# Performance work log

Measured on AMD Instinct MI355X. Metric: run time of the kernel, lower is better.

## Reference

```python
import jax, jax.numpy as jnp
import numpy as np

N_NODES = 100000
N_EDGES = 1600000
HID = 256
HEADS = 4
HEAD_DIM = HID // HEADS
EPS = 1e-5


def _layernorm(x, g, b):
    mu = jnp.mean(x, axis=-1, keepdims=True)
    var = jnp.mean(jnp.square(x - mu), axis=-1, keepdims=True)
    return (x - mu) * jax.lax.rsqrt(var + EPS) * g + b


def setup_inputs() -> dict:
    key = jax.random.key(0)
    ks = jax.random.split(key, 16)
    s = 0.05  # small init, mimics xavier gain=0.1
    inp = {
        'h': jax.random.normal(ks[0], (N_NODES, HID), jnp.float32),
        'src': jax.random.randint(ks[1], (N_EDGES,), 0, N_NODES, jnp.int32),
        'dst': jax.random.randint(ks[2], (N_EDGES,), 0, N_NODES, jnp.int32),
        'Wq': jax.random.normal(ks[3], (HID, HID), jnp.float32) * s,
        'bq': jnp.zeros((HID,), jnp.float32),
        'Wk': jax.random.normal(ks[4], (HID, HID), jnp.float32) * s,
        'bk': jnp.zeros((HID,), jnp.float32),
        'Wv': jax.random.normal(ks[5], (HID, HID), jnp.float32) * s,
        'bv': jnp.zeros((HID,), jnp.float32),
        'Wo': jax.random.normal(ks[6], (HID, HID), jnp.float32) * s,
        'bo': jnp.zeros((HID,), jnp.float32),
        'W1': jax.random.normal(ks[7], (HID, 2 * HID), jnp.float32) * s,
        'b1': jnp.zeros((2 * HID,), jnp.float32),
        'W2': jax.random.normal(ks[8], (2 * HID, HID), jnp.float32) * s,
        'b2': jnp.zeros((HID,), jnp.float32),
        'g1': jnp.ones((HID,), jnp.float32),
        'be1': jnp.zeros((HID,), jnp.float32),
        'g2': jnp.ones((HID,), jnp.float32),
        'be2': jnp.zeros((HID,), jnp.float32),
    }
    return inp


def reference(h, src, dst, Wq, bq, Wk, bk, Wv, bv, Wo, bo, W1, b1, W2, b2, g1, be1, g2, be2):
    N = h.shape[0]
    scale = HEAD_DIM ** -0.5
    h_norm = _layernorm(h, g1, be1)
    Q = (h_norm @ Wq + bq).reshape(N, HEADS, HEAD_DIM)
    K = (h_norm @ Wk + bk).reshape(N, HEADS, HEAD_DIM)
    V = (h_norm @ Wv + bv).reshape(N, HEADS, HEAD_DIM)

    # per-edge attention logits: q from dst, k from src  -> [E, heads]
    logits = jnp.einsum('ehd,ehd->eh', Q[dst], K[src]) * scale

    # edge softmax grouped by destination node (dgl.ops.edge_softmax)
    seg_max = jax.ops.segment_max(logits, dst, num_segments=N)  # [N, heads]
    e = jnp.exp(logits - seg_max[dst])
    seg_sum = jax.ops.segment_sum(e, dst, num_segments=N)
    w = e / seg_sum[dst]  # [E, heads]

    # message = V[src] * attn ; aggregate by sum over incoming edges
    msg = V[src] * w[:, :, None]  # [E, heads, head_dim]
    h_new = jax.ops.segment_sum(msg, dst, num_segments=N).reshape(N, HID)

    h_attn = h_new @ Wo + bo
    h = h + h_attn  # dropout is identity in eval
    h2 = _layernorm(h, g2, be2)
    ffn = jax.nn.relu(h2 @ W1 + b1) @ W2 + b2
    return h + ffn
```

## Files before the change

### kernel.cpp

```cpp
#include <hip/hip_runtime.h>
#include <hip/hip_bf16.h>

#define NN 100000
#define NE 1600000

typedef __attribute__((ext_vector_type(8))) short bf16x8;
typedef __attribute__((ext_vector_type(4))) float f32x4;
typedef __attribute__((ext_vector_type(2))) float f32x2;
typedef __attribute__((ext_vector_type(2))) unsigned int u32x2;
typedef __attribute__((ext_vector_type(4))) unsigned int u32x4;

__device__ __forceinline__ float bf2f(unsigned short u) {
    union { unsigned int i; float f; } c; c.i = ((unsigned int)u) << 16; return c.f;
}
__device__ __forceinline__ unsigned short f2bf(float f) {
    union { float f; unsigned int i; } c; c.f = f;
    unsigned int lsb = (c.i >> 16) & 1u;
    c.i += 0x7FFFu + lsb;
    return (unsigned short)(c.i >> 16);
}
__device__ __forceinline__ u32x4 pack8bf(f32x4 a, f32x4 b) {
    u32x4 p;
    p.x = f2bf(a[0]) | ((unsigned int)f2bf(a[1]) << 16);
    p.y = f2bf(a[2]) | ((unsigned int)f2bf(a[3]) << 16);
    p.z = f2bf(b[0]) | ((unsigned int)f2bf(b[1]) << 16);
    p.w = f2bf(b[2]) | ((unsigned int)f2bf(b[3]) << 16);
    return p;
}
__device__ __forceinline__ void gload_lds16(const void* g, void* l) {
    __builtin_amdgcn_global_load_lds(
        (const __attribute__((address_space(1))) void*)g,
        (__attribute__((address_space(3))) void*)l, 16, 0, 0);
}

__global__ __launch_bounds__(256) void ln_k(
    const float* __restrict__ x, const float* __restrict__ g,
    const float* __restrict__ b, unsigned short* __restrict__ y, int nrows)
{
    int w = threadIdx.x >> 6, lane = threadIdx.x & 63;
    int row = blockIdx.x * 4 + w;
    if (row >= nrows) return;
    const float4 xv = *(const float4*)(x + (size_t)row * 256 + lane * 4);
    float s  = xv.x + xv.y + xv.z + xv.w;
    float sq = xv.x*xv.x + xv.y*xv.y + xv.z*xv.z + xv.w*xv.w;
    #pragma unroll
    for (int m = 1; m < 64; m <<= 1) {
        s  += __shfl_xor(s,  m);
        sq += __shfl_xor(sq, m);
    }
    float mu  = s * (1.0f / 256.0f);
    float var = sq * (1.0f / 256.0f) - mu * mu;
    float r = rsqrtf(var + 1e-5f);
    float4 gv = *(const float4*)(g + lane * 4);
    float4 bv = *(const float4*)(b + lane * 4);
    ushort4 o;
    o.x = f2bf((xv.x - mu) * r * gv.x + bv.x);
    o.y = f2bf((xv.y - mu) * r * gv.y + bv.y);
    o.z = f2bf((xv.z - mu) * r * gv.z + bv.z);
    o.w = f2bf((xv.w - mu) * r * gv.w + bv.w);
    *(ushort4*)(y + (size_t)row * 256 + lane * 4) = o;
}

__global__ __launch_bounds__(256) void wconv_k(
    const float* __restrict__ W, unsigned short* __restrict__ Wt, int K, int N)
{
    __shared__ unsigned short tl[32][33];
    int bk = blockIdx.x * 32, bn = blockIdx.y * 32;
    int lx = threadIdx.x & 31, ly = threadIdx.x >> 5;
    #pragma unroll
    for (int r = 0; r < 32; r += 8)
        tl[ly + r][lx] = f2bf(W[(size_t)(bk + ly + r) * N + bn + lx]);
    __syncthreads();
    #pragma unroll
    for (int r = 0; r < 32; r += 8)
        Wt[(size_t)(bn + ly + r) * K + bk + lx] = tl[lx][ly + r];
}

__global__ void bcat_k(const float* __restrict__ a, const float* __restrict__ b,
                       const float* __restrict__ c, float* __restrict__ o)
{
    int t = threadIdx.x;
    o[t] = a[t]; o[256 + t] = b[t]; o[512 + t] = c[t];
}

template<int OMODE, bool RELU, bool RES>
__global__ __launch_bounds__(512) void mgemm_k(
    const unsigned short* __restrict__ A, const unsigned short* __restrict__ Wt,
    const float* __restrict__ bias, void* __restrict__ outv, void* __restrict__ out2,
    const void* __restrict__ res, const float* __restrict__ g, const float* __restrict__ be,
    int M, int N, int K)
{
    __shared__ __align__(16) char lds[49152];
    const int t = threadIdx.x;
    const int lane = t & 63;
    const int wid = t >> 6;
    const int wm = wid >> 2, wn = wid & 3;
    const int bm = blockIdx.y * 128, bn = blockIdx.x * 256;

    f32x4 acc[4][4] = {};

    const int ra_s = t >> 2;
    const int sa_s = (t & 3) ^ (ra_s & 3);
    const size_t arow = (size_t)min(bm + ra_s, M - 1) * K + sa_s * 8;
    const int rb0 = t >> 2;
    const int sb0 = (t & 3) ^ (rb0 & 3);
    const int rb1 = (512 + t) >> 2;
    const int sb1 = (t & 3) ^ (rb1 & 3);
    const size_t brow0 = (size_t)(bn + rb0) * K + sb0 * 8;
    const size_t brow1 = (size_t)(bn + rb1) * K + sb1 * 8;

    const int fr = lane & 15, fs = lane >> 4;
    const int rslot = fs ^ (fr & 3);

    const int KS = K >> 5;
    int cur = 0;
    {
        unsigned short* Ab = (unsigned short*)(lds);
        unsigned short* Bb = (unsigned short*)(lds + 16384);
        gload_lds16(A + arow, Ab + t * 8);
        gload_lds16(Wt + brow0, Bb + t * 8);
        gload_lds16(Wt + brow1, Bb + (512 + t) * 8);
    }
    for (int ks = 0; ks < KS; ++ks) {
        __syncthreads();
        if (ks + 1 < KS) {
            int k1 = (ks + 1) << 5;
            unsigned short* Ab = (unsigned short*)(lds + (cur ^ 1) * 8192);
            unsigned short* Bb = (unsigned short*)(lds + 16384 + (cur ^ 1) * 16384);
            gload_lds16(A + arow + k1, Ab + t * 8);
            gload_lds16(Wt + brow0 + k1, Bb + t * 8);
            gload_lds16(Wt + brow1 + k1, Bb + (512 + t) * 8);
        }
        const unsigned short* As = (const unsigned short*)(lds + cur * 8192);
        const unsigned short* Bs = (const unsigned short*)(lds + 16384 + cur * 16384);
        bf16x8 af[4], bf[4];
        #pragma unroll
        for (int fm = 0; fm < 4; ++fm)
            af[fm] = *(const bf16x8*)&As[(wm * 64 + fm * 16 + fr) * 32 + rslot * 8];
        #pragma unroll
        for (int fn = 0; fn < 4; ++fn)
            bf[fn] = *(const bf16x8*)&Bs[(wn * 64 + fn * 16 + fr) * 32 + rslot * 8];
        #pragma unroll
        for (int fm = 0; fm < 4; ++fm)
            #pragma unroll
            for (int fn = 0; fn < 4; ++fn)
                acc[fm][fn] = __builtin_amdgcn_mfma_f32_16x16x32_bf16(
                    af[fm], bf[fn], acc[fm][fn], 0, 0, 0);
        cur ^= 1;
    }
    __syncthreads();

    float* wl = (float*)(lds + wid * 4352);
    float* stats = (float*)(lds + 34816);
    const int rr = lane >> 2;
    const int c4 = (lane & 3) * 16;
    const int qg = lane >> 4;

    #pragma unroll
    for (int fm = 0; fm < 4; ++fm) {
        #pragma unroll
        for (int fn = 0; fn < 4; ++fn)
            #pragma unroll
            for (int i = 0; i < 4; ++i)
                wl[(qg * 4 + i) * 68 + fn * 16 + fr] = acc[fm][fn][i];
        f32x4 v0 = *(const f32x4*)&wl[rr * 68 + c4 + 0];
        f32x4 v1 = *(const f32x4*)&wl[rr * 68 + c4 + 4];
        f32x4 v2 = *(const f32x4*)&wl[rr * 68 + c4 + 8];
        f32x4 v3 = *(const f32x4*)&wl[rr * 68 + c4 + 12];
        const int rowg = bm + wm * 64 + fm * 16 + rr;
        const int colg = bn + wn * 64 + c4;
        if (rowg < M) {
            v0 += *(const f32x4*)&bias[colg + 0];
            v1 += *(const f32x4*)&bias[colg + 4];
            v2 += *(const f32x4*)&bias[colg + 8];
            v3 += *(const f32x4*)&bias[colg + 12];
            if (RES) {
                if (OMODE == 4) {
                    const unsigned short* rp = (const unsigned short*)res + (size_t)rowg * N + colg;
                    u32x4 ra = *(const u32x4*)rp;
                    u32x4 rb = *(const u32x4*)(rp + 8);
                    v0[0] += bf2f(ra.x & 0xffff); v0[1] += bf2f(ra.x >> 16);
                    v0[2] += bf2f(ra.y & 0xffff); v0[3] += bf2f(ra.y >> 16);
                    v1[0] += bf2f(ra.z & 0xffff); v1[1] += bf2f(ra.z >> 16);
                    v1[2] += bf2f(ra.w & 0xffff); v1[3] += bf2f(ra.w >> 16);
                    v2[0] += bf2f(rb.x & 0xffff); v2[1] += bf2f(rb.x >> 16);
                    v2[2] += bf2f(rb.y & 0xffff); v2[3] += bf2f(rb.y >> 16);
                    v3[0] += bf2f(rb.z & 0xffff); v3[1] += bf2f(rb.z >> 16);
                    v3[2] += bf2f(rb.w & 0xffff); v3[3] += bf2f(rb.w >> 16);
                } else {
                    const float* rp = (const float*)res + (size_t)rowg * N + colg;
                    v0 += *(const f32x4*)(rp + 0);
                    v1 += *(const f32x4*)(rp + 4);
                    v2 += *(const f32x4*)(rp + 8);
                    v3 += *(const f32x4*)(rp + 12);
                }
            }
            if (RELU) {
                #pragma unroll
                for (int j = 0; j < 4; ++j) {
                    v0[j] = fmaxf(v0[j], 0.f); v1[j] = fmaxf(v1[j], 0.f);
                    v2[j] = fmaxf(v2[j], 0.f); v3[j] = fmaxf(v3[j], 0.f);
                }
            }
        } else {
            v0 = 0.f; v1 = 0.f; v2 = 0.f; v3 = 0.f;
        }

        if (OMODE == 3) {
            acc[fm][0] = v0; acc[fm][1] = v1; acc[fm][2] = v2; acc[fm][3] = v3;
        } else if (rowg < M) {
            if (OMODE == 0 || OMODE == 4) {
                float* op = (float*)outv + (size_t)rowg * N + colg;
                *(f32x4*)(op + 0) = v0; *(f32x4*)(op + 4) = v1;
                *(f32x4*)(op + 8) = v2; *(f32x4*)(op + 12) = v3;
            } else if (OMODE == 1) {
                unsigned short* op = (unsigned short*)outv + (size_t)rowg * N + colg;
                *(u32x4*)(op + 0) = pack8bf(v0, v1);
                *(u32x4*)(op + 8) = pack8bf(v2, v3);
            } else {
                if (colg < 256) {
                    unsigned short* op = (unsigned short*)outv + (size_t)rowg * 256 + colg;
                    *(u32x4*)(op + 0) = pack8bf(v0, v1);
                    *(u32x4*)(op + 8) = pack8bf(v2, v3);
                } else {
                    u32x4 p8;
                    unsigned int w0, w1, w2, w3;
                    w0 = __builtin_amdgcn_cvt_pk_fp8_f32(v0[0], v0[1], 0, false);
                    w0 = __builtin_amdgcn_cvt_pk_fp8_f32(v0[2], v0[3], w0, true);
                    w1 = __builtin_amdgcn_cvt_pk_fp8_f32(v1[0], v1[1], 0, false);
                    w1 = __builtin_amdgcn_cvt_pk_fp8_f32(v1[2], v1[3], w1, true);
                    w2 = __builtin_amdgcn_cvt_pk_fp8_f32(v2[0], v2[1], 0, false);
                    w2 = __builtin_amdgcn_cvt_pk_fp8_f32(v2[2], v2[3], w2, true);
                    w3 = __builtin_amdgcn_cvt_pk_fp8_f32(v3[0], v3[1], 0, false);
                    w3 = __builtin_amdgcn_cvt_pk_fp8_f32(v3[2], v3[3], w3, true);
                    p8.x = w0; p8.y = w1; p8.z = w2; p8.w = w3;
                    *(u32x4*)((unsigned char*)out2 + (size_t)rowg * 512 + (colg - 256)) = p8;
                }
            }
        }
    }

    if (OMODE == 3) {
        #pragma unroll
        for (int fm = 0; fm < 4; ++fm) {
            float s = 0.f, q = 0.f;
            #pragma unroll
            for (int j = 0; j < 4; ++j)
                #pragma unroll
                for (int c = 0; c < 4; ++c) {
                    float x = acc[fm][j][c];
                    s += x; q += x * x;
                }
            s += __shfl_xor(s, 1); q += __shfl_xor(q, 1);
            s += __shfl_xor(s, 2); q += __shfl_xor(q, 2);
            if ((lane & 3) == 0) {
                int rowl = wm * 64 + fm * 16 + rr;
                stats[rowl * 8 + wn * 2 + 0] = s;
                stats[rowl * 8 + wn * 2 + 1] = q;
            }
        }
        __syncthreads();
        #pragma unroll
        for (int fm = 0; fm < 4; ++fm) {
            const int rowl = wm * 64 + fm * 16 + rr;
            const int rowg = bm + rowl;
            float s = stats[rowl * 8 + 0] + stats[rowl * 8 + 2] + stats[rowl * 8 + 4] + stats[rowl * 8 + 6];
            float q = stats[rowl * 8 + 1] + stats[rowl * 8 + 3] + stats[rowl * 8 + 5] + stats[rowl * 8 + 7];
            float mu = s * (1.0f / 256.0f);
            float var = q * (1.0f / 256.0f) - mu * mu;
            float rstd = rsqrtf(var + 1e-5f);
            const int colg = bn + wn * 64 + c4;
            if (rowg < M) {
                unsigned short* mp = (unsigned short*)out2 + (size_t)rowg * 256 + colg;
                *(u32x4*)(mp + 0) = pack8bf(acc[fm][0], acc[fm][1]);
                *(u32x4*)(mp + 8) = pack8bf(acc[fm][2], acc[fm][3]);
                f32x4 nv[4];
                #pragma unroll
                for (int j = 0; j < 4; ++j) {
                    f32x4 gv = *(const f32x4*)&g[colg + j * 4];
                    f32x4 bv = *(const f32x4*)&be[colg + j * 4];
                    #pragma unroll
                    for (int c = 0; c < 4; ++c)
                        nv[j][c] = (acc[fm][j][c] - mu) * rstd * gv[c] + bv[c];
                }
                unsigned short* op = (unsigned short*)outv + (size_t)rowg * 256 + colg;
                *(u32x4*)(op + 0) = pack8bf(nv[0], nv[1]);
                *(u32x4*)(op + 8) = pack8bf(nv[2], nv[3]);
            }
        }
    }
}

__global__ void degcnt_k(const int* __restrict__ dst, int* __restrict__ deg, int E)
{
    int e = blockIdx.x * blockDim.x + threadIdx.x;
    if (e < E) atomicAdd(deg + dst[e], 1);
}

__global__ __launch_bounds__(1024) void scan_k(int* __restrict__ a, int n)
{
    __shared__ int wsum[16];
    __shared__ int carry;
    __shared__ int tot;
    int t = threadIdx.x, lane = t & 63, w = t >> 6;
    if (t == 0) carry = 0;
    __syncthreads();
    for (int base = 0; base < n; base += 1024) {
        int i = base + t;
        int v = (i < n) ? a[i] : 0;
        int s = v;
        #pragma unroll
        for (int d2 = 1; d2 < 64; d2 <<= 1) {
            int u = __shfl_up(s, d2);
            if (lane >= d2) s += u;
        }
        if (lane == 63) wsum[w] = s;
        __syncthreads();
        if (t == 0) {
            int run = 0;
            #pragma unroll
            for (int j = 0; j < 16; ++j) { int x = wsum[j]; wsum[j] = run; run += x; }
            tot = run;
        }
        __syncthreads();
        int excl = carry + wsum[w] + (s - v);
        if (i < n) a[i] = excl;
        __syncthreads();
        if (t == 0) carry += tot;
        __syncthreads();
    }
    if (threadIdx.x == 0) a[n] = carry;
}

__global__ void scatter_k(
    const int* __restrict__ dst, const int* __restrict__ srcarr,
    const int* __restrict__ off, int* __restrict__ cursor,
    int* __restrict__ csr, int E)
{
    int e = blockIdx.x * blockDim.x + threadIdx.x;
    if (e >= E) return;
    int d = dst[e];
    int pos = off[d] + atomicAdd(cursor + d, 1);
    csr[pos] = srcarr[e];
}

__global__ __launch_bounds__(256) void attn_k(
    const int* __restrict__ csr, const int* __restrict__ off,
    const unsigned short* __restrict__ Q, const unsigned char* __restrict__ KV8,
    unsigned short* __restrict__ hnew)
{
    int w = threadIdx.x >> 6, lane = threadIdx.x & 63;
    int n = blockIdx.x * 4 + w;
    if (n >= NN) return;
    int e0 = off[n], e1 = off[n + 1];

    u32x2 qr = __builtin_nontemporal_load((const u32x2*)(Q + (size_t)n * 256 + lane * 4));
    const float q0 = bf2f((unsigned short)(qr.x & 0xffff)) * 0.125f;
    const float q1 = bf2f((unsigned short)(qr.x >> 16))    * 0.125f;
    const float q2 = bf2f((unsigned short)(qr.y & 0xffff)) * 0.125f;
    const float q3 = bf2f((unsigned short)(qr.y >> 16))    * 0.125f;

    float s = 0.f;
    float a0 = 0.f, a1 = 0.f, a2 = 0.f, a3 = 0.f;

    int i = e0;
    for (; i + 7 < e1; i += 8) {
        int ns[8];
        #pragma unroll
        for (int j = 0; j < 8; ++j) ns[j] = csr[i + j];
        unsigned int kd[8], vd[8];
        #pragma unroll
        for (int j = 0; j < 8; ++j) {
            const unsigned char* r = KV8 + (size_t)ns[j] * 512 + lane * 4;
            kd[j] = *(const unsigned int*)r;
            vd[j] = *(const unsigned int*)(r + 256);
        }
        float l[8];
        #pragma unroll
        for (int j = 0; j < 8; ++j) {
            f32x2 ka = __builtin_amdgcn_cvt_pk_f32_fp8(kd[j], false);
            f32x2 kb = __builtin_amdgcn_cvt_pk_f32_fp8(kd[j], true);
            l[j] = q0 * ka.x + q1 * ka.y + q2 * kb.x + q3 * kb.y;
        }
        #pragma unroll
        for (int m2 = 1; m2 < 16; m2 <<= 1) {
            #pragma unroll
            for (int j = 0; j < 8; ++j) l[j] += __shfl_xor(l[j], m2);
        }
        #pragma unroll
        for (int j = 0; j < 8; ++j) {
            float p = __expf(l[j]);
            f32x2 va = __builtin_amdgcn_cvt_pk_f32_fp8(vd[j], false);
            f32x2 vb = __builtin_amdgcn_cvt_pk_f32_fp8(vd[j], true);
            s  += p;
            a0 += p * va.x; a1 += p * va.y;
            a2 += p * vb.x; a3 += p * vb.y;
        }
    }
    for (; i + 3 < e1; i += 4) {
        int ns[4];
        #pragma unroll
        for (int j = 0; j < 4; ++j) ns[j] = csr[i + j];
        unsigned int kd[4], vd[4];
        #pragma unroll
        for (int j = 0; j < 4; ++j) {
            const unsigned char* r = KV8 + (size_t)ns[j] * 512 + lane * 4;
            kd[j] = *(const unsigned int*)r;
            vd[j] = *(const unsigned int*)(r + 256);
        }
        float l[4];
        #pragma unroll
        for (int j = 0; j < 4; ++j) {
            f32x2 ka = __builtin_amdgcn_cvt_pk_f32_fp8(kd[j], false);
            f32x2 kb = __builtin_amdgcn_cvt_pk_f32_fp8(kd[j], true);
            l[j] = q0 * ka.x + q1 * ka.y + q2 * kb.x + q3 * kb.y;
        }
        #pragma unroll
        for (int m2 = 1; m2 < 16; m2 <<= 1) {
            #pragma unroll
            for (int j = 0; j < 4; ++j) l[j] += __shfl_xor(l[j], m2);
        }
        #pragma unroll
        for (int j = 0; j < 4; ++j) {
            float p = __expf(l[j]);
            f32x2 va = __builtin_amdgcn_cvt_pk_f32_fp8(vd[j], false);
            f32x2 vb = __builtin_amdgcn_cvt_pk_f32_fp8(vd[j], true);
            s  += p;
            a0 += p * va.x; a1 += p * va.y;
            a2 += p * vb.x; a3 += p * vb.y;
        }
    }
    for (; i < e1; ++i) {
        int n0 = csr[i];
        const unsigned char* r = KV8 + (size_t)n0 * 512 + lane * 4;
        unsigned int kd = *(const unsigned int*)r;
        unsigned int vd = *(const unsigned int*)(r + 256);
        f32x2 ka = __builtin_amdgcn_cvt_pk_f32_fp8(kd, false);
        f32x2 kb = __builtin_amdgcn_cvt_pk_f32_fp8(kd, true);
        float l0 = q0 * ka.x + q1 * ka.y + q2 * kb.x + q3 * kb.y;
        #pragma unroll
        for (int m2 = 1; m2 < 16; m2 <<= 1) l0 += __shfl_xor(l0, m2);
        float p = __expf(l0);
        f32x2 va = __builtin_amdgcn_cvt_pk_f32_fp8(vd, false);
        f32x2 vb = __builtin_amdgcn_cvt_pk_f32_fp8(vd, true);
        s  += p;
        a0 += p * va.x; a1 += p * va.y;
        a2 += p * vb.x; a3 += p * vb.y;
    }
    float inv = (e1 > e0) ? 1.0f / s : 0.f;
    u32x2 ov;
    ov.x = ((unsigned int)f2bf(a1 * inv) << 16) | f2bf(a0 * inv);
    ov.y = ((unsigned int)f2bf(a3 * inv) << 16) | f2bf(a2 * inv);
    __builtin_nontemporal_store(ov, (u32x2*)(hnew + (size_t)n * 256 + lane * 4));
}

extern "C" void kernel_launch(void* const* d_in, const int* in_sizes, int n_in,
                              void* d_out, int out_size, void* d_ws, size_t ws_size,
                              hipStream_t stream)
{
    if (n_in < 19) return;
    const float* h   = (const float*)d_in[0];
    const int*   src = (const int*)d_in[1];
    const int*   dst = (const int*)d_in[2];
    const float* Wq  = (const float*)d_in[3];
    const float* bq  = (const float*)d_in[4];
    const float* Wk  = (const float*)d_in[5];
    const float* bk  = (const float*)d_in[6];
    const float* Wv  = (const float*)d_in[7];
    const float* bv  = (const float*)d_in[8];
    const float* Wo  = (const float*)d_in[9];
    const float* bo  = (const float*)d_in[10];
    const float* W1  = (const float*)d_in[11];
    const float* b1  = (const float*)d_in[12];
    const float* W2  = (const float*)d_in[13];
    const float* b2  = (const float*)d_in[14];
    const float* g1  = (const float*)d_in[15];
    const float* be1 = (const float*)d_in[16];
    const float* g2  = (const float*)d_in[17];
    const float* be2 = (const float*)d_in[18];
    float* out = (float*)d_out;

    char* w = (char*)d_ws;
    unsigned short* hnormb = (unsigned short*)(w + 0);
    unsigned short* Qb     = (unsigned short*)(w + 51200000);
    unsigned char*  KV8    = (unsigned char*)(w + 102400000);
    int*            degoff = (int*)(w + 153600000);
    int*            cursor = (int*)(w + 154000384);
    int*            csr    = (int*)(w + 154400768);
    unsigned short* Wqkvt  = (unsigned short*)(w + 204800000);
    unsigned short* Wot    = (unsigned short*)(w + 205193216);
    unsigned short* W1t    = (unsigned short*)(w + 205324288);
    unsigned short* W2t    = (unsigned short*)(w + 205586432);
    float*          bqkv   = (float*)(w + 205848576);
    unsigned short* hnewb  = hnormb;
    unsigned short* h2nb   = hnormb;
    unsigned short* hmidb  = Qb;
    unsigned short* ffnmid = (unsigned short*)(w + 102400000);

    hipMemsetAsync(degoff, 0, 400384, stream);
    hipMemsetAsync(cursor, 0, 400384, stream);

    const int M = NN;
    dim3 blk(256);
    dim3 blk512(512);

    wconv_k<<<dim3(8, 8),  blk, 0, stream>>>(Wq, Wqkvt,             256, 256);
    wconv_k<<<dim3(8, 8),  blk, 0, stream>>>(Wk, Wqkvt + 256 * 256, 256, 256);
    wconv_k<<<dim3(8, 8),  blk, 0, stream>>>(Wv, Wqkvt + 512 * 256, 256, 256);
    wconv_k<<<dim3(8, 8),  blk, 0, stream>>>(Wo, Wot, 256, 256);
    wconv_k<<<dim3(8, 16), blk, 0, stream>>>(W1, W1t, 256, 512);
    wconv_k<<<dim3(16, 8), blk, 0, stream>>>(W2, W2t, 512, 256);
    bcat_k<<<dim3(1), blk, 0, stream>>>(bq, bk, bv, bqkv);

    degcnt_k<<<dim3((NE + 255) / 256), blk, 0, stream>>>(dst, degoff, NE);
    scan_k<<<dim3(1), dim3(1024), 0, stream>>>(degoff, NN);
    scatter_k<<<dim3((NE + 255) / 256), blk, 0, stream>>>(dst, src, degoff, cursor, csr, NE);

    ln_k<<<dim3((NN + 3) / 4), blk, 0, stream>>>(h, g1, be1, hnormb, NN);

    dim3 gq(768 / 256, (M + 127) / 128);
    mgemm_k<2, false, false><<<gq, blk512, 0, stream>>>(hnormb, Wqkvt, bqkv, Qb, KV8, nullptr, nullptr, nullptr, M, 768, 256);

    attn_k<<<dim3((NN + 3) / 4), blk, 0, stream>>>(csr, degoff, Qb, KV8, hnewb);

    dim3 go(1, (M + 127) / 128);
    mgemm_k<3, false, true><<<go, blk512, 0, stream>>>(hnewb, Wot, bo, h2nb, hmidb, h, g2, be2, M, 256, 256);

    dim3 g1x(512 / 256, (M + 127) / 128);
    mgemm_k<1, true, false><<<g1x, blk512, 0, stream>>>(h2nb, W1t, b1, ffnmid, nullptr, nullptr, nullptr, nullptr, M, 512, 256);
    mgemm_k<4, false, true><<<go, blk512, 0, stream>>>(ffnmid, W2t, b2, out, nullptr, hmidb, nullptr, nullptr, M, 256, 512);
}
```

Before: 684.2 us.

## Load GEMM fragments directly from global, parallelize scan, fuse weight conversions

The GEMM drops its LDS double-buffered staging: each wave now reads its MFMA fragments straight from global memory with a compile-time K loop that is fully unrolled. It also gains a launch-bounds occupancy hint and keeps LDS only for the epilogue. The single-block degree scan becomes a three-kernel multi-block scan, and the six weight-transpose launches plus the bias concat are merged into one kernel. In attention, the CSR entries are stored as pre-shifted byte offsets and exp is replaced by exp2 with log2(e) folded into the query scale. The risk is that global fragment loads lose the shared reuse across waves and may be less coalesced, which could make the GEMMs more bandwidth-bound.

```diff
diff --git a/kernel.cpp b/kernel.cpp
--- a/kernel.cpp
+++ b/kernel.cpp
@@ -26,11 +26,6 @@
     p.z = f2bf(b[0]) | ((unsigned int)f2bf(b[1]) << 16);
     p.w = f2bf(b[2]) | ((unsigned int)f2bf(b[3]) << 16);
     return p;
-}
-__device__ __forceinline__ void gload_lds16(const void* g, void* l) {
-    __builtin_amdgcn_global_load_lds(
-        (const __attribute__((address_space(1))) void*)g,
-        (__attribute__((address_space(3))) void*)l, 16, 0, 0);
 }
 
 __global__ __launch_bounds__(256) void ln_k(
@@ -61,94 +56,86 @@
     *(ushort4*)(y + (size_t)row * 256 + lane * 4) = o;
 }
 
-__global__ __launch_bounds__(256) void wconv_k(
-    const float* __restrict__ W, unsigned short* __restrict__ Wt, int K, int N)
-{
+__global__ __launch_bounds__(256) void wcv_all_k(
+    const float* __restrict__ Wq, const float* __restrict__ Wk, const float* __restrict__ Wv,
+    const float* __restrict__ Wo, const float* __restrict__ W1, const float* __restrict__ W2,
+    unsigned short* __restrict__ Wqkvt, unsigned short* __restrict__ Wot,
+    unsigned short* __restrict__ W1t, unsigned short* __restrict__ W2t,
+    const float* __restrict__ bq, const float* __restrict__ bk, const float* __restrict__ bv,
+    float* __restrict__ bqkv)
+{
+    int id = blockIdx.x;
+    int t = threadIdx.x;
+    if (id == 512) {
+        bqkv[t] = bq[t]; bqkv[256 + t] = bk[t]; bqkv[512 + t] = bv[t];
+        return;
+    }
+    const float* W; unsigned short* Wt; int K, N, kx, ny;
+    if (id < 192) {
+        int grp = id >> 6, l = id & 63;
+        W = (grp == 0) ? Wq : ((grp == 1) ? Wk : Wv);
+        Wt = Wqkvt + grp * 256 * 256;
+        K = 256; N = 256; kx = l & 7; ny = l >> 3;
+    } else if (id < 256) {
+        int l = id - 192; W = Wo; Wt = Wot; K = 256; N = 256; kx = l & 7; ny = l >> 3;
+    } else if (id < 384) {
+        int l = id - 256; W = W1; Wt = W1t; K = 256; N = 512; kx = l & 7; ny = l >> 3;
+    } else {
+        int l = id - 384; W = W2; Wt = W2t; K = 512; N = 256; kx = l & 15; ny = l >> 4;
+    }
     __shared__ unsigned short tl[32][33];
-    int bk = blockIdx.x * 32, bn = blockIdx.y * 32;
-    int lx = threadIdx.x & 31, ly = threadIdx.x >> 5;
+    int bk2 = kx * 32, bn = ny * 32;
+    int lx = t & 31, ly = t >> 5;
     #pragma unroll
     for (int r = 0; r < 32; r += 8)
-        tl[ly + r][lx] = f2bf(W[(size_t)(bk + ly + r) * N + bn + lx]);
+        tl[ly + r][lx] = f2bf(W[(size_t)(bk2 + ly + r) * N + bn + lx]);
     __syncthreads();
     #pragma unroll
     for (int r = 0; r < 32; r += 8)
-        Wt[(size_t)(bn + ly + r) * K + bk + lx] = tl[lx][ly + r];
-}
-
-__global__ void bcat_k(const float* __restrict__ a, const float* __restrict__ b,
-                       const float* __restrict__ c, float* __restrict__ o)
-{
-    int t = threadIdx.x;
-    o[t] = a[t]; o[256 + t] = b[t]; o[512 + t] = c[t];
-}
-
-template<int OMODE, bool RELU, bool RES>
-__global__ __launch_bounds__(512) void mgemm_k(
+        Wt[(size_t)(bn + ly + r) * K + bk2 + lx] = tl[lx][ly + r];
+}
+
+template<int KS, int OMODE, bool RELU, bool RES>
+__global__ __launch_bounds__(512, 4) void mgemm_k(
     const unsigned short* __restrict__ A, const unsigned short* __restrict__ Wt,
     const float* __restrict__ bias, void* __restrict__ outv, void* __restrict__ out2,
     const void* __restrict__ res, const float* __restrict__ g, const float* __restrict__ be,
-    int M, int N, int K)
-{
-    __shared__ __align__(16) char lds[49152];
+    int M, int N)
+{
+    constexpr int K = KS * 32;
+    __shared__ __align__(16) char lds[38912];
     const int t = threadIdx.x;
     const int lane = t & 63;
     const int wid = t >> 6;
     const int wm = wid >> 2, wn = wid & 3;
     const int bm = blockIdx.y * 128, bn = blockIdx.x * 256;
+    const int fr = lane & 15, fs = lane >> 4;
 
     f32x4 acc[4][4] = {};
 
-    const int ra_s = t >> 2;
-    const int sa_s = (t & 3) ^ (ra_s & 3);
-    const size_t arow = (size_t)min(bm + ra_s, M - 1) * K + sa_s * 8;
-    const int rb0 = t >> 2;
-    const int sb0 = (t & 3) ^ (rb0 & 3);
-    const int rb1 = (512 + t) >> 2;
-    const int sb1 = (t & 3) ^ (rb1 & 3);
-    const size_t brow0 = (size_t)(bn + rb0) * K + sb0 * 8;
-    const size_t brow1 = (size_t)(bn + rb1) * K + sb1 * 8;
-
-    const int fr = lane & 15, fs = lane >> 4;
-    const int rslot = fs ^ (fr & 3);
-
-    const int KS = K >> 5;
-    int cur = 0;
-    {
-        unsigned short* Ab = (unsigned short*)(lds);
-        unsigned short* Bb = (unsigned short*)(lds + 16384);
-        gload_lds16(A + arow, Ab + t * 8);
-        gload_lds16(Wt + brow0, Bb + t * 8);
-        gload_lds16(Wt + brow1, Bb + (512 + t) * 8);
-    }
+    const unsigned short* Ap[4];
+    const unsigned short* Bp[4];
+    #pragma unroll
+    for (int fm = 0; fm < 4; ++fm)
+        Ap[fm] = A + (size_t)min(bm + wm * 64 + fm * 16 + fr, M - 1) * K + fs * 8;
+    #pragma unroll
+    for (int fn = 0; fn < 4; ++fn)
+        Bp[fn] = Wt + (size_t)(bn + wn * 64 + fn * 16 + fr) * K + fs * 8;
+
+    #pragma unroll
     for (int ks = 0; ks < KS; ++ks) {
-        __syncthreads();
-        if (ks + 1 < KS) {
-            int k1 = (ks + 1) << 5;
-            unsigned short* Ab = (unsigned short*)(lds + (cur ^ 1) * 8192);
-            unsigned short* Bb = (unsigned short*)(lds + 16384 + (cur ^ 1) * 16384);
-            gload_lds16(A + arow + k1, Ab + t * 8);
-            gload_lds16(Wt + brow0 + k1, Bb + t * 8);
-            gload_lds16(Wt + brow1 + k1, Bb + (512 + t) * 8);
-        }
-        const unsigned short* As = (const unsigned short*)(lds + cur * 8192);
-        const unsigned short* Bs = (const unsigned short*)(lds + 16384 + cur * 16384);
         bf16x8 af[4], bf[4];
         #pragma unroll
-        for (int fm = 0; fm < 4; ++fm)
-            af[fm] = *(const bf16x8*)&As[(wm * 64 + fm * 16 + fr) * 32 + rslot * 8];
-        #pragma unroll
-        for (int fn = 0; fn < 4; ++fn)
-            bf[fn] = *(const bf16x8*)&Bs[(wn * 64 + fn * 16 + fr) * 32 + rslot * 8];
+        for (int fm = 0; fm < 4; ++fm) af[fm] = *(const bf16x8*)(Ap[fm] + ks * 32);
+        #pragma unroll
+        for (int fn = 0; fn < 4; ++fn) bf[fn] = *(const bf16x8*)(Bp[fn] + ks * 32);
         #pragma unroll
         for (int fm = 0; fm < 4; ++fm)
             #pragma unroll
             for (int fn = 0; fn < 4; ++fn)
                 acc[fm][fn] = __builtin_amdgcn_mfma_f32_16x16x32_bf16(
                     af[fm], bf[fn], acc[fm][fn], 0, 0, 0);
-        cur ^= 1;
-    }
-    __syncthreads();
+    }
 
     float* wl = (float*)(lds + wid * 4352);
     float* stats = (float*)(lds + 34816);
@@ -163,6 +150,7 @@
             #pragma unroll
             for (int i = 0; i < 4; ++i)
                 wl[(qg * 4 + i) * 68 + fn * 16 + fr] = acc[fm][fn][i];
+        __builtin_amdgcn_s_waitcnt(0);
         f32x4 v0 = *(const f32x4*)&wl[rr * 68 + c4 + 0];
         f32x4 v1 = *(const f32x4*)&wl[rr * 68 + c4 + 4];
         f32x4 v2 = *(const f32x4*)&wl[rr * 68 + c4 + 8];
@@ -297,39 +285,53 @@
     if (e < E) atomicAdd(deg + dst[e], 1);
 }
 
-__global__ __launch_bounds__(1024) void scan_k(int* __restrict__ a, int n)
+__global__ __launch_bounds__(1024) void scanA_k(int* __restrict__ a, int* __restrict__ aux, int n)
 {
     __shared__ int wsum[16];
-    __shared__ int carry;
-    __shared__ int tot;
+    __shared__ int wpre[16];
     int t = threadIdx.x, lane = t & 63, w = t >> 6;
-    if (t == 0) carry = 0;
+    int i = blockIdx.x * 1024 + t;
+    int v = (i < n) ? a[i] : 0;
+    int s = v;
+    #pragma unroll
+    for (int d = 1; d < 64; d <<= 1) {
+        int u = __shfl_up(s, d);
+        if (lane >= d) s += u;
+    }
+    if (lane == 63) wsum[w] = s;
     __syncthreads();
-    for (int base = 0; base < n; base += 1024) {
-        int i = base + t;
-        int v = (i < n) ? a[i] : 0;
-        int s = v;
-        #pragma unroll
-        for (int d2 = 1; d2 < 64; d2 <<= 1) {
-            int u = __shfl_up(s, d2);
-            if (lane >= d2) s += u;
-        }
-        if (lane == 63) wsum[w] = s;
-        __syncthreads();
-        if (t == 0) {
-            int run = 0;
-            #pragma unroll
-            for (int j = 0; j < 16; ++j) { int x = wsum[j]; wsum[j] = run; run += x; }
-            tot = run;
-        }
-        __syncthreads();
-        int excl = carry + wsum[w] + (s - v);
-        if (i < n) a[i] = excl;
-        __syncthreads();
-        if (t == 0) carry += tot;
-        __syncthreads();
-    }
-    if (threadIdx.x == 0) a[n] = carry;
+    if (t == 0) {
+        int run = 0;
+        #pragma unroll
+        for (int j = 0; j < 16; ++j) { wpre[j] = run; run += wsum[j]; }
+        aux[blockIdx.x] = run;
+    }
+    __syncthreads();
+    if (i < n) a[i] = wpre[w] + s - v;
+}
+
+__global__ __launch_bounds__(128) void scanB_k(int* __restrict__ aux, int* __restrict__ tot, int nb)
+{
+    __shared__ int ws[2];
+    int t = threadIdx.x, lane = t & 63, w = t >> 6;
+    int v = (t < nb) ? aux[t] : 0;
+    int s = v;
+    #pragma unroll
+    for (int d = 1; d < 64; d <<= 1) {
+        int u = __shfl_up(s, d);
+        if (lane >= d) s += u;
+    }
+    if (lane == 63) ws[w] = s;
+    __syncthreads();
+    int add = (w == 1) ? ws[0] : 0;
+    if (t < nb) aux[t] = add + s - v;
+    if (t == nb - 1) tot[0] = add + s;
+}
+
+__global__ __launch_bounds__(1024) void scanC_k(int* __restrict__ a, const int* __restrict__ aux, int n)
+{
+    int i = blockIdx.x * 1024 + threadIdx.x;
+    if (i < n) a[i] += aux[blockIdx.x];
 }
 
 __global__ void scatter_k(
@@ -341,7 +343,7 @@
     if (e >= E) return;
     int d = dst[e];
     int pos = off[d] + atomicAdd(cursor + d, 1);
-    csr[pos] = srcarr[e];
+    csr[pos] = srcarr[e] << 9;
 }
 
 __global__ __launch_bounds__(256) void attn_k(
@@ -354,11 +356,14 @@
     if (n >= NN) return;
     int e0 = off[n], e1 = off[n + 1];
 
+    const unsigned char* KVl = KV8 + lane * 4;
+
     u32x2 qr = __builtin_nontemporal_load((const u32x2*)(Q + (size_t)n * 256 + lane * 4));
-    const float q0 = bf2f((unsigned short)(qr.x & 0xffff)) * 0.125f;
-    const float q1 = bf2f((unsigned short)(qr.x >> 16))    * 0.125f;
-    const float q2 = bf2f((unsigned short)(qr.y & 0xffff)) * 0.125f;
-    const float q3 = bf2f((unsigned short)(qr.y >> 16))    * 0.125f;
+    const float qs = 0.125f * 1.4426950408889634f;
+    const float q0 = bf2f((unsigned short)(qr.x & 0xffff)) * qs;
+    const float q1 = bf2f((unsigned short)(qr.x >> 16))    * qs;
+    const float q2 = bf2f((unsigned short)(qr.y & 0xffff)) * qs;
+    const float q3 = bf2f((unsigned short)(qr.y >> 16))    * qs;
 
     float s = 0.f;
     float a0 = 0.f, a1 = 0.f, a2 = 0.f, a3 = 0.f;
@@ -371,7 +376,7 @@
         unsigned int kd[8], vd[8];
         #pragma unroll
         for (int j = 0; j < 8; ++j) {
-            const unsigned char* r = KV8 + (size_t)ns[j] * 512 + lane * 4;
+            const unsigned char* r = KVl + (size_t)(unsigned)ns[j];
             kd[j] = *(const unsigned int*)r;
             vd[j] = *(const unsigned int*)(r + 256);
         }
@@ -389,7 +394,7 @@
         }
         #pragma unroll
         for (int j = 0; j < 8; ++j) {
-            float p = __expf(l[j]);
+            float p = exp2f(l[j]);
             f32x2 va = __builtin_amdgcn_cvt_pk_f32_fp8(vd[j], false);
             f32x2 vb = __builtin_amdgcn_cvt_pk_f32_fp8(vd[j], true);
             s  += p;
@@ -404,7 +409,7 @@
         unsigned int kd[4], vd[4];
         #pragma unroll
         for (int j = 0; j < 4; ++j) {
-            const unsigned char* r = KV8 + (size_t)ns[j] * 512 + lane * 4;
+            const unsigned char* r = KVl + (size_t)(unsigned)ns[j];
             kd[j] = *(const unsigned int*)r;
             vd[j] = *(const unsigned int*)(r + 256);
         }
@@ -422,7 +427,7 @@
         }
         #pragma unroll
         for (int j = 0; j < 4; ++j) {
-            float p = __expf(l[j]);
+            float p = exp2f(l[j]);
             f32x2 va = __builtin_amdgcn_cvt_pk_f32_fp8(vd[j], false);
             f32x2 vb = __builtin_amdgcn_cvt_pk_f32_fp8(vd[j], true);
             s  += p;
@@ -431,8 +436,7 @@
         }
     }
     for (; i < e1; ++i) {
-        int n0 = csr[i];
-        const unsigned char* r = KV8 + (size_t)n0 * 512 + lane * 4;
+        const unsigned char* r = KVl + (size_t)(unsigned)csr[i];
         unsigned int kd = *(const unsigned int*)r;
         unsigned int vd = *(const unsigned int*)(r + 256);
         f32x2 ka = __builtin_amdgcn_cvt_pk_f32_fp8(kd, false);
@@ -440,7 +444,7 @@
         float l0 = q0 * ka.x + q1 * ka.y + q2 * kb.x + q3 * kb.y;
         #pragma unroll
         for (int m2 = 1; m2 < 16; m2 <<= 1) l0 += __shfl_xor(l0, m2);
-        float p = __expf(l0);
+        float p = exp2f(l0);
         f32x2 va = __builtin_amdgcn_cvt_pk_f32_fp8(vd, false);
         f32x2 vb = __builtin_amdgcn_cvt_pk_f32_fp8(vd, true);
         s  += p;
@@ -492,6 +496,7 @@
     unsigned short* W1t    = (unsigned short*)(w + 205324288);
     unsigned short* W2t    = (unsigned short*)(w + 205586432);
     float*          bqkv   = (float*)(w + 205848576);
+    int*            scanaux= (int*)(w + 205851648);
     unsigned short* hnewb  = hnormb;
     unsigned short* h2nb   = hnormb;
     unsigned short* hmidb  = Qb;
@@ -503,30 +508,28 @@
     const int M = NN;
     dim3 blk(256);
     dim3 blk512(512);
-
-    wconv_k<<<dim3(8, 8),  blk, 0, stream>>>(Wq, Wqkvt,             256, 256);
-    wconv_k<<<dim3(8, 8),  blk, 0, stream>>>(Wk, Wqkvt + 256 * 256, 256, 256);
-    wconv_k<<<dim3(8, 8),  blk, 0, stream>>>(Wv, Wqkvt + 512 * 256, 256, 256);
-    wconv_k<<<dim3(8, 8),  blk, 0, stream>>>(Wo, Wot, 256, 256);
-    wconv_k<<<dim3(8, 16), blk, 0, stream>>>(W1, W1t, 256, 512);
-    wconv_k<<<dim3(16, 8), blk, 0, stream>>>(W2, W2t, 512, 256);
-    bcat_k<<<dim3(1), blk, 0, stream>>>(bq, bk, bv, bqkv);
+    const int SCAN_BLKS = (NN + 1023) / 1024;
+
+    wcv_all_k<<<dim3(513), blk, 0, stream>>>(Wq, Wk, Wv, Wo, W1, W2,
+                                             Wqkvt, Wot, W1t, W2t, bq, bk, bv, bqkv);
 
     degcnt_k<<<dim3((NE + 255) / 256), blk, 0, stream>>>(dst, degoff, NE);
-    scan_k<<<dim3(1), dim3(1024), 0, stream>>>(degoff, NN);
+    scanA_k<<<dim3(SCAN_BLKS), dim3(1024), 0, stream>>>(degoff, scanaux, NN);
+    scanB_k<<<dim3(1), dim3(128), 0, stream>>>(scanaux, degoff + NN, SCAN_BLKS);
+    scanC_k<<<dim3(SCAN_BLKS), dim3(1024), 0, stream>>>(degoff, scanaux, NN);
     scatter_k<<<dim3((NE + 255) / 256), blk, 0, stream>>>(dst, src, degoff, cursor, csr, NE);
 
     ln_k<<<dim3((NN + 3) / 4), blk, 0, stream>>>(h, g1, be1, hnormb, NN);
 
-    dim3 gq(768 / 256, (M + 127) / 128);
-    mgemm_k<2, false, false><<<gq, blk512, 0, stream>>>(hnormb, Wqkvt, bqkv, Qb, KV8, nullptr, nullptr, nullptr, M, 768, 256);
+    dim3 gq(3, (M + 127) / 128);
+    mgemm_k<8, 2, false, false><<<gq, blk512, 0, stream>>>(hnormb, Wqkvt, bqkv, Qb, KV8, nullptr, nullptr, nullptr, M, 768);
 
     attn_k<<<dim3((NN + 3) / 4), blk, 0, stream>>>(csr, degoff, Qb, KV8, hnewb);
 
     dim3 go(1, (M + 127) / 128);
-    mgemm_k<3, false, true><<<go, blk512, 0, stream>>>(hnewb, Wot, bo, h2nb, hmidb, h, g2, be2, M, 256, 256);
-
-    dim3 g1x(512 / 256, (M + 127) / 128);
-    mgemm_k<1, true, false><<<g1x, blk512, 0, stream>>>(h2nb, W1t, b1, ffnmid, nullptr, nullptr, nullptr, nullptr, M, 512, 256);
-    mgemm_k<4, false, true><<<go, blk512, 0, stream>>>(ffnmid, W2t, b2, out, nullptr, hmidb, nullptr, nullptr, M, 256, 512);
-}
+    mgemm_k<8, 3, false, true><<<go, blk512, 0, stream>>>(hnewb, Wot, bo, h2nb, hmidb, h, g2, be2, M, 256);
+
+    dim3 g1x(2, (M + 127) / 128);
+    mgemm_k<8, 1, true, false><<<g1x, blk512, 0, stream>>>(h2nb, W1t, b1, ffnmid, nullptr, nullptr, nullptr, nullptr, M, 512);
+    mgemm_k<16, 4, false, true><<<go, blk512, 0, stream>>>(ffnmid, W2t, b2, out, nullptr, hmidb, nullptr, nullptr, M, 256);
+}
```

Result: slower. 874.8 us (+27.9%).
